# Kernel optimization log

Measured on AMD Instinct MI355X. Metric: run time of the kernel, lower is better.

## Reference

```python
import jax, jax.numpy as jnp
import numpy as np

VOCAB = 32000
DIM = 256
LAYERS = 2
CLASSES = 8
BATCH = 32
SEQ = 8192


def setup_inputs() -> dict:
    key = jax.random.key(0)
    ks = jax.random.split(key, 8)
    s = 1.0 / np.sqrt(DIM)
    x = jax.random.randint(ks[0], (BATCH, SEQ), 0, VOCAB, dtype=jnp.int32)
    emb = jax.random.normal(ks[1], (VOCAB, DIM), dtype=jnp.float32)
    Wz = jax.random.normal(ks[2], (LAYERS, DIM, DIM), dtype=jnp.float32) * s
    bz = jnp.zeros((LAYERS, DIM), dtype=jnp.float32)
    Wh = jax.random.normal(ks[3], (LAYERS, DIM, DIM), dtype=jnp.float32) * s
    bh = jnp.zeros((LAYERS, DIM), dtype=jnp.float32)
    Wo = jax.random.normal(ks[4], (DIM, CLASSES), dtype=jnp.float32) * s
    bo = jnp.zeros((CLASSES,), dtype=jnp.float32)
    return {"x": x, "emb": emb, "Wz": Wz, "bz": bz, "Wh": Wh, "bh": bh, "Wo": Wo, "bo": bo}


def _min_gru_layer(h_in, Wz_l, bz_l, Wh_l, bh_l):
    # minGRU: z_t = sigmoid(W_z x_t); h~_t = W_h x_t
    # h_t = (1 - z_t) * h_{t-1} + z_t * h~_t,  h_0 = 0
    z = jax.nn.sigmoid(jnp.einsum('bsd,de->bse', h_in, Wz_l) + bz_l)
    h_tilde = jnp.einsum('bsd,de->bse', h_in, Wh_l) + bh_l
    a = 1.0 - z          # decay coefficient
    b = z * h_tilde      # input contribution
    # parallel associative scan of h_t = a_t * h_{t-1} + b_t (h_0 = 0)
    def combine(c1, c2):
        a1, b1 = c1
        a2, b2 = c2
        return a1 * a2, b1 * a2 + b2
    _, h = jax.lax.associative_scan(combine, (a, b), axis=1)
    return h


def reference(x, emb, Wz, bz, Wh, bh, Wo, bo):
    h = emb[x]  # [B, S, D]
    for l in range(LAYERS):
        h = _min_gru_layer(h, Wz[l], bz[l], Wh[l], bh[l])
    # classifier on the last timestep
    return h[:, -1] @ Wo + bo  # [B, CLASSES]
```

## Files before the change

### kernel.cpp

```cpp
#include <hip/hip_runtime.h>
#include <stdint.h>

#define SEQ 8192
#define CS 64
#define NCH 128
#define HB2 16
#define HBLK (HB2 * NCH)

typedef float f32x4 __attribute__((ext_vector_type(4)));
typedef short short8 __attribute__((ext_vector_type(8)));
typedef unsigned short u16;
typedef u16 ushort8 __attribute__((ext_vector_type(8)));
typedef u16 ushort4v __attribute__((ext_vector_type(4)));
typedef uint32_t uint4v __attribute__((ext_vector_type(4)));

__device__ __forceinline__ u16 f2bf(float f) {
  uint32_t u = __float_as_uint(f);
  u += 0x7fffu + ((u >> 16) & 1u);
  return (u16)(u >> 16);
}
__device__ __forceinline__ float bf2f(uint32_t lo16) {
  return __uint_as_float(lo16 << 16);
}

__device__ __forceinline__ void gld16(void* lds, const void* g) {
  __builtin_amdgcn_global_load_lds(
      (const __attribute__((address_space(1))) uint32_t*)g,
      (__attribute__((address_space(3))) uint32_t*)lds, 16, 0, 0);
}

__global__ void embq_kernel(const float* __restrict__ emb, u16* __restrict__ embq) {
  int i = (blockIdx.x * 256 + threadIdx.x) * 4;
  float4 v = *(const float4*)(emb + i);
  ushort4v p;
  p[0] = f2bf(v.x); p[1] = f2bf(v.y); p[2] = f2bf(v.z); p[3] = f2bf(v.w);
  *(ushort4v*)(embq + i) = p;
}

__global__ void wt_kernel(const float* __restrict__ Wz, const float* __restrict__ Wh,
                          u16* __restrict__ WtS) {
  int idx = blockIdx.x * 256 + threadIdx.x;
  int d = idx & 255;
  int k = (idx >> 8) & 255;
  int m = idx >> 16;
  const float* src = (m < 2 ? Wz : Wh) + (size_t)(m & 1) * 65536;
  float v = src[k * 256 + d];
  int dh = d >> 6, dloc = d & 63, k32 = k >> 5, kl = k & 31;
  size_t tile = ((size_t)(m * 4 + dh) * 8 + k32) * 4096;
  size_t byte = (size_t)(dloc * 64 + ((kl * 2) ^ (((dloc >> 1) & 3) << 4)));
  *(u16*)((char*)WtS + tile + byte) = f2bf(v);
}

__device__ __forceinline__ void stage32(char* dst_wave, const char* WtSb, int mat, int k32,
                                        int w, int lane) {
  const char* src = WtSb + ((size_t)((mat * 4 + w) * 8 + k32)) * 4096 + lane * 16;
  #pragma unroll
  for (int i = 0; i < 4; i++)
    gld16(dst_wave + i * 1024, src + i * 1024);
}

__device__ __forceinline__ void load_fa(const u16* As, int k32, int l15, int lg,
                                        short8 (&fa)[4]) {
  const int xm = (l15 & 7) << 4;
  const int kt = k32 >> 1, ks = k32 & 1;
  #pragma unroll
  for (int mi = 0; mi < 4; mi++)
    fa[mi] = *(const short8*)((const char*)As + kt * 8192 +
               (((mi * 16 + l15) * 128 + ks * 64 + lg * 16) ^ xm));
}

__device__ __forceinline__ void mfma_frags(const char* Pw, const short8 (&fa)[4],
    int l15, int lg, f32x4 (&acc)[4][4])
{
  #pragma unroll
  for (int ni = 0; ni < 4; ni++) {
    const int dloc = ni * 16 + l15;
    const int off = dloc * 64 + ((lg * 16) ^ (((dloc >> 1) & 3) << 4));
    short8 fb = *(const short8*)(Pw + off);
    #pragma unroll
    for (int mi = 0; mi < 4; mi++)
      acc[mi][ni] = __builtin_amdgcn_mfma_f32_16x16x32_bf16(fa[mi], fb, acc[mi][ni], 0, 0, 0);
  }
}

__device__ __forceinline__ void gemm_pipe3(int lsel, const char* WtSb, const u16* As,
    char* Pw, int w, int l15, int lg, int lane,
    f32x4 (&accz)[4][4], f32x4 (&acch)[4][4])
{
  stage32(Pw,         WtSb, lsel,     0, w, lane);
  stage32(Pw + 16384, WtSb, 2 + lsel, 0, w, lane);
  short8 fa[4];
  #pragma unroll
  for (int i = 0; i < 16; ++i) {
    if (i < 15) asm volatile("s_waitcnt vmcnt(4)" ::: "memory");
    else        asm volatile("s_waitcnt vmcnt(0)" ::: "memory");
    __builtin_amdgcn_sched_barrier(0);
    if (i + 2 < 16)
      stage32(Pw + ((i + 2) % 3) * 16384, WtSb,
              ((i + 2) & 1) ? (2 + lsel) : lsel, (i + 2) >> 1, w, lane);
    if ((i & 1) == 0) {
      load_fa(As, i >> 1, l15, lg, fa);
      mfma_frags(Pw + (i % 3) * 16384, fa, l15, lg, accz);
    } else {
      mfma_frags(Pw + (i % 3) * 16384, fa, l15, lg, acch);
    }
  }
}

__device__ __forceinline__ float2* seg_ptr(char* segt, int s, int d) {
  return (float2*)(segt + s * 2048 + ((d * 8) ^ (s << 4)));
}


template<int PHASE>
__global__ __launch_bounds__(256, 2)
void gru_kernel(const int* __restrict__ x, const u16* __restrict__ embq,
                const u16* __restrict__ WtS,
                const float* __restrict__ bz0, const float* __restrict__ bh0,
                const float* __restrict__ bz1, const float* __restrict__ bh1,
                const float* __restrict__ carry, uint32_t* __restrict__ ab,
                float* __restrict__ Ap, float* __restrict__ Bs)
{
  __shared__ __align__(16) u16 As[16384];
  __shared__ __align__(16) char Pb[49152];

  const int tid = threadIdx.x;
  const int lane = tid & 63;
  const int w = tid >> 6;
  const int l15 = lane & 15, lg = lane >> 4;
  const int cb = blockIdx.x;
  const int b = cb >> 7, c = cb & (NCH - 1);
  const char* WtSb = (const char*)WtS;
  char* segt = (char*)As;
  char* Pw = Pb + w * 4096;

  f32x4 accz[4][4], acch[4][4];
  #pragma unroll
  for (int i = 0; i < 4; i++)
    #pragma unroll
    for (int j = 0; j < 4; j++) {
      f32x4 zz = {0.f, 0.f, 0.f, 0.f};
      accz[i][j] = zz; acch[i][j] = zz;
    }

  if (PHASE == 0) {
    {
      const int sm = tid >> 2, kq = tid & 3;
      const int tok = x[b * SEQ + c * CS + sm];
      const u16* src = embq + (size_t)tok * 256 + kq * 64;
      char* sub = (char*)As + kq * 8192;
      const int swz = (sm & 7) << 4;
      #pragma unroll
      for (int j = 0; j < 8; j++) {
        ushort8 p = *(const ushort8*)(src + j * 8);
        *(ushort8*)(sub + ((sm * 128 + j * 16) ^ swz)) = p;
      }
    }
    __syncthreads();
    gemm_pipe3(0, WtSb, As, Pw, w, l15, lg, lane, accz, acch);
    __syncthreads();

    #pragma unroll
    for (int ni = 0; ni < 4; ni++) {
      const int d = w * 64 + ni * 16 + l15;
      const float bzv = bz0[d];
      const float bhv = bh0[d];
      #pragma unroll
      for (int mi = 0; mi < 4; mi++) {
        float A = 1.f, B = 0.f;
        uint4v pk4;
        #pragma unroll
        for (int r = 0; r < 4; r++) {
          float zl = accz[mi][ni][r] + bzv;
          float a = __builtin_amdgcn_rcpf(1.f + __expf(zl));
          float ht = acch[mi][ni][r] + bhv;
          float bb = (1.f - a) * ht;
          pk4[r] = (uint32_t)f2bf(a) | ((uint32_t)f2bf(bb) << 16);
          B = B * a + bb;
          A *= a;
        }
        *(uint4v*)(ab + (size_t)cb * 16384 +
                   (size_t)((mi * 16 + ni * 4 + w) * 256 + (lg * 16 + l15) * 4)) = pk4;
        *seg_ptr(segt, mi * 4 + lg, d) = make_float2(A, B);
      }
    }
    __syncthreads();
    {
      float PA = 1.f, PB = 0.f;
      #pragma unroll
      for (int s = 0; s < 16; s++) {
        float2 v = *seg_ptr(segt, s, tid);
        PB = v.x * PB + v.y;
        PA *= v.x;
      }
      Ap[(size_t)cb * 256 + tid] = PA;
      Bs[(size_t)cb * 256 + tid] = PB;
    }
    return;
  }

  {
    const int d = tid;
    const int wq = d >> 6, niq = (d >> 4) & 3, l15q = d & 15;
    float h = carry[(size_t)cb * 256 + d];
    const uint32_t* pab = ab + (size_t)cb * 16384 +
                          (size_t)((niq * 4 + wq) * 256 + l15q * 4);
    char* sub = (char*)As + wq * 8192;
    const int kl2 = (d & 63) * 2;
    #pragma unroll
    for (int mi = 0; mi < 4; mi++) {
      #pragma unroll
      for (int lgq = 0; lgq < 4; lgq++) {
        uint4v u4 = *(const uint4v*)(pab + mi * 4096 + lgq * 64);
        #pragma unroll
        for (int r = 0; r < 4; r++) {
          uint32_t u = u4[r];
          h = bf2f(u & 0xffffu) * h + bf2f(u >> 16);
          const int t = mi * 16 + lgq * 4 + r;
          *(u16*)(sub + ((t * 128 + kl2) ^ ((t & 7) << 4))) = f2bf(h);
        }
      }
    }
  }
  __syncthreads();
  gemm_pipe3(1, WtSb, As, Pw, w, l15, lg, lane, accz, acch);
  __syncthreads();

  #pragma unroll
  for (int ni = 0; ni < 4; ni++) {
    const int d = w * 64 + ni * 16 + l15;
    const float bzv = bz1[d];
    const float bhv = bh1[d];
    #pragma unroll
    for (int mi = 0; mi < 4; mi++) {
      float A = 1.f, B = 0.f;
      #pragma unroll
      for (int r = 0; r < 4; r++) {
        float zl = accz[mi][ni][r] + bzv;
        float a = __builtin_amdgcn_rcpf(1.f + __expf(zl));
        float ht = acch[mi][ni][r] + bhv;
        float bb = (1.f - a) * ht;
        B = B * a + bb;
        A *= a;
      }
      *seg_ptr(segt, mi * 4 + lg, d) = make_float2(A, B);
    }
  }
  __syncthreads();
  {
    float PA = 1.f, PB = 0.f;
    #pragma unroll
    for (int s = 0; s < 16; s++) {
      float2 v = *seg_ptr(segt, s, tid);
      PB = v.x * PB + v.y;
      PA *= v.x;
    }
    Ap[(size_t)cb * 256 + tid] = PA;
    Bs[(size_t)cb * 256 + tid] = PB;
  }
}

__global__ void scan2_l0(const float* __restrict__ Ap0, const float* __restrict__ Bs0,
                         float* __restrict__ carry) {
  const int g = blockIdx.x * 256 + threadIdx.x;
  const int b = g >> 8, d = g & 255;
  float h = 0.f;
  for (int c = 0; c < NCH; c++) {
    const size_t idx = (size_t)(b * NCH + c) * 256 + d;
    carry[idx] = h;
    h = Bs0[idx] + Ap0[idx] * h;
  }
}

__global__ void scan2_l1(const float* __restrict__ Ap1, const float* __restrict__ Bs1,
                         float* __restrict__ hlast) {
  const int g = blockIdx.x * 256 + threadIdx.x;
  const int b = g >> 8, d = g & 255;
  float h = 0.f;
  for (int c = 0; c < NCH; c++) {
    const size_t idx = (size_t)(b * NCH + c) * 256 + d;
    h = Bs1[idx] + Ap1[idx] * h;
  }
  hlast[b * 256 + d] = h;
}

__global__ void cls_kernel(const float* __restrict__ hlast, const float* __restrict__ Wo,
                           const float* __restrict__ bo, float* __restrict__ out) {
  const int t = threadIdx.x;
  const int b = t >> 3, c = t & 7;
  float acc = bo[c];
  for (int d = 0; d < 256; d++) acc += hlast[b * 256 + d] * Wo[d * 8 + c];
  out[t] = acc;
}

extern "C" void kernel_launch(void* const* d_in, const int* in_sizes, int n_in,
                              void* d_out, int out_size, void* d_ws, size_t ws_size,
                              hipStream_t stream) {
  (void)in_sizes; (void)n_in; (void)out_size; (void)ws_size;
  const int*   x   = (const int*)d_in[0];
  const float* emb = (const float*)d_in[1];
  const float* Wz  = (const float*)d_in[2];
  const float* bz  = (const float*)d_in[3];
  const float* Wh  = (const float*)d_in[4];
  const float* bh  = (const float*)d_in[5];
  const float* Wo  = (const float*)d_in[6];
  const float* bo  = (const float*)d_in[7];
  float* out = (float*)d_out;
  char* ws = (char*)d_ws;

  u16*      embq  = (u16*)     (ws);
  u16*      WtS   = (u16*)     (ws + 16777216ull);
  float*    Ap0   = (float*)   (ws + 17301504ull);
  float*    Bs0   = (float*)   (ws + 19398656ull);
  float*    carry = (float*)   (ws + 21495808ull);
  float*    Ap1   = (float*)   (ws + 23592960ull);
  float*    Bs1   = (float*)   (ws + 27787264ull);
  float*    hlast = (float*)   (ws + 31981568ull);
  uint32_t* ab    = (uint32_t*)(ws + 32014336ull);

  embq_kernel<<<8000, 256, 0, stream>>>(emb, embq);
  wt_kernel<<<1024, 256, 0, stream>>>(Wz, Wh, WtS);

  for (int hf = 0; hf < 2; hf++) {
    const int* xh = x + (size_t)hf * HB2 * SEQ;
    gru_kernel<0><<<HBLK, 256, 0, stream>>>(
        xh, embq, WtS, bz, bh, bz + 256, bh + 256, nullptr, ab, Ap0, Bs0);
    scan2_l0<<<HB2, 256, 0, stream>>>(Ap0, Bs0, carry);
    gru_kernel<1><<<HBLK, 256, 0, stream>>>(
        xh, embq, WtS, bz, bh, bz + 256, bh + 256, carry, ab,
        Ap1 + (size_t)hf * HBLK * 256, Bs1 + (size_t)hf * HBLK * 256);
  }

  scan2_l1<<<32, 256, 0, stream>>>(Ap1, Bs1, hlast);
  cls_kernel<<<1, 256, 0, stream>>>(hlast, Wo, bo, out);
}
```

Measured before the change: 261.3 us.

## Store chunk-prefix scan coefficients so layer-1 carry apply is parallel per timestep

The first phase now computes full in-chunk prefix (A,B) coefficients for every timestep. It uses an exclusive scan over the 16 segments, written back into shared memory, and stores these prefix pairs in bf16 instead of the raw per-step (a,b). The second phase then forms each h_t independently as A_t*carry + B_t, with each thread handling its own fragment positions. This removes the serial 64-step dependent recurrence per channel in the apply pass. In exchange it adds an extra barrier and prefix work in the first phase, and the bf16 rounding now falls on cumulative products rather than per-step values.

```diff
diff --git a/kernel.cpp b/kernel.cpp
--- a/kernel.cpp
+++ b/kernel.cpp
@@ -168,57 +168,75 @@
       #pragma unroll
       for (int mi = 0; mi < 4; mi++) {
         float A = 1.f, B = 0.f;
-        uint4v pk4;
         #pragma unroll
         for (int r = 0; r < 4; r++) {
           float zl = accz[mi][ni][r] + bzv;
           float a = __builtin_amdgcn_rcpf(1.f + __expf(zl));
           float ht = acch[mi][ni][r] + bhv;
           float bb = (1.f - a) * ht;
-          pk4[r] = (uint32_t)f2bf(a) | ((uint32_t)f2bf(bb) << 16);
+          accz[mi][ni][r] = a; acch[mi][ni][r] = bb;
           B = B * a + bb;
           A *= a;
         }
+        *seg_ptr(segt, mi * 4 + lg, d) = make_float2(A, B);
+      }
+    }
+    __syncthreads();
+
+    {
+      float PA = 1.f, PB = 0.f;
+      #pragma unroll
+      for (int s = 0; s < 16; s++) {
+        float2* p = seg_ptr(segt, s, tid);
+        float2 v = *p;
+        *p = make_float2(PA, PB);
+        PB = v.x * PB + v.y;
+        PA *= v.x;
+      }
+      Ap[(size_t)cb * 256 + tid] = PA;
+      Bs[(size_t)cb * 256 + tid] = PB;
+    }
+    __syncthreads();
+
+    #pragma unroll
+    for (int ni = 0; ni < 4; ni++) {
+      const int d = w * 64 + ni * 16 + l15;
+      #pragma unroll
+      for (int mi = 0; mi < 4; mi++) {
+        float2 e = *seg_ptr(segt, mi * 4 + lg, d);
+        float Ar = 1.f, Br = 0.f;
+        uint4v pk4;
+        #pragma unroll
+        for (int r = 0; r < 4; r++) {
+          Br = Br * accz[mi][ni][r] + acch[mi][ni][r];
+          Ar *= accz[mi][ni][r];
+          float Ai = Ar * e.x;
+          float Bi = Ar * e.y + Br;
+          pk4[r] = (uint32_t)f2bf(Ai) | ((uint32_t)f2bf(Bi) << 16);
+        }
         *(uint4v*)(ab + (size_t)cb * 16384 +
                    (size_t)((mi * 16 + ni * 4 + w) * 256 + (lg * 16 + l15) * 4)) = pk4;
-        *seg_ptr(segt, mi * 4 + lg, d) = make_float2(A, B);
-      }
-    }
-    __syncthreads();
-    {
-      float PA = 1.f, PB = 0.f;
-      #pragma unroll
-      for (int s = 0; s < 16; s++) {
-        float2 v = *seg_ptr(segt, s, tid);
-        PB = v.x * PB + v.y;
-        PA *= v.x;
-      }
-      Ap[(size_t)cb * 256 + tid] = PA;
-      Bs[(size_t)cb * 256 + tid] = PB;
+      }
     }
     return;
   }
 
-  {
-    const int d = tid;
-    const int wq = d >> 6, niq = (d >> 4) & 3, l15q = d & 15;
-    float h = carry[(size_t)cb * 256 + d];
-    const uint32_t* pab = ab + (size_t)cb * 16384 +
-                          (size_t)((niq * 4 + wq) * 256 + l15q * 4);
-    char* sub = (char*)As + wq * 8192;
+  #pragma unroll
+  for (int ni = 0; ni < 4; ni++) {
+    const int d = w * 64 + ni * 16 + l15;
+    const float h0 = carry[(size_t)cb * 256 + d];
+    char* sub = (char*)As + (d >> 6) * 8192;
     const int kl2 = (d & 63) * 2;
     #pragma unroll
     for (int mi = 0; mi < 4; mi++) {
-      #pragma unroll
-      for (int lgq = 0; lgq < 4; lgq++) {
-        uint4v u4 = *(const uint4v*)(pab + mi * 4096 + lgq * 64);
-        #pragma unroll
-        for (int r = 0; r < 4; r++) {
-          uint32_t u = u4[r];
-          h = bf2f(u & 0xffffu) * h + bf2f(u >> 16);
-          const int t = mi * 16 + lgq * 4 + r;
-          *(u16*)(sub + ((t * 128 + kl2) ^ ((t & 7) << 4))) = f2bf(h);
-        }
+      uint4v u4 = *(const uint4v*)(ab + (size_t)cb * 16384 +
+                   (size_t)((mi * 16 + ni * 4 + w) * 256 + (lg * 16 + l15) * 4));
+      #pragma unroll
+      for (int r = 0; r < 4; r++) {
+        uint32_t u = u4[r];
+        float h = bf2f(u & 0xffffu) * h0 + bf2f(u >> 16);
+        const int t = mi * 16 + lg * 4 + r;
+        *(u16*)(sub + ((t * 128 + kl2) ^ ((t & 7) << 4))) = f2bf(h);
       }
     }
   }
```

Result: slower. 270.1 us (+3.4%).
